# Kernel tuning notes

Measured on AMD Instinct MI355X. Metric: run time of the kernel, lower is better.

Reference implementation:

```python
import jax, jax.numpy as jnp
import numpy as np

N_NODES = 50000
N_EDGES = 800000
N_GRAPHS = 256
F_IN, HID, EMB = 128, 256, 128
N_GROUPS, N_FAM = 16, 128


def setup_inputs() -> dict:
    key = jax.random.key(0)
    ks = jax.random.split(key, 12)
    x = jax.random.normal(ks[0], (N_NODES, F_IN), dtype=jnp.float32)
    edge_index = jax.random.randint(ks[1], (2, N_EDGES), 0, N_NODES, dtype=jnp.int64)
    batch = jnp.sort(jax.random.randint(ks[2], (N_NODES,), 0, N_GRAPHS, dtype=jnp.int64))
    def lin(k, fi, fo):
        s = 1.0 / np.sqrt(fi)
        return jax.random.uniform(k, (fi, fo), minval=-s, maxval=s, dtype=jnp.float32)
    W1 = lin(ks[3], F_IN, HID); b1 = jnp.zeros((HID,), jnp.float32)
    W2 = lin(ks[4], HID, EMB); b2 = jnp.zeros((EMB,), jnp.float32)
    Wg = lin(ks[5], EMB, N_GROUPS); bg = jnp.zeros((N_GROUPS,), jnp.float32)
    s = 1.0 / np.sqrt(EMB)
    Wf = jax.random.uniform(ks[6], (N_GROUPS, EMB, N_FAM), minval=-s, maxval=s, dtype=jnp.float32)
    bf = jnp.zeros((N_GROUPS, N_FAM), jnp.float32)
    return {"x": x, "edge_index": edge_index, "batch": batch,
            "W1": W1, "b1": b1, "W2": W2, "b2": b2,
            "Wg": Wg, "bg": bg, "Wf": Wf, "bf": bf}


def _gcn_conv(h, src, dst, coef, W, b, n):
    # h: [N, Fin]; src/dst: [E'] (self-loops included); coef: [E'] sym-norm
    hw = h @ W                                    # [N, Fout]
    msg = hw[src] * coef[:, None]                 # gather + scale, [E', Fout]
    out = jax.ops.segment_sum(msg, dst, num_segments=n)  # scatter-add
    return out + b


def reference(x, edge_index, batch, W1, b1, W2, b2, Wg, bg, Wf, bf):
    n = x.shape[0]
    loops = jnp.arange(n, dtype=edge_index.dtype)
    src = jnp.concatenate([edge_index[0], loops])
    dst = jnp.concatenate([edge_index[1], loops])
    # symmetric GCN normalization (deg >= 1 thanks to self-loops)
    deg = jax.ops.segment_sum(jnp.ones_like(dst, dtype=x.dtype), dst, num_segments=n)
    dinv = jax.lax.rsqrt(deg)
    coef = dinv[src] * dinv[dst]

    h1 = jax.nn.relu(_gcn_conv(x, src, dst, coef, W1, b1, n))  # dropout = identity (eval)
    h2 = _gcn_conv(h1, src, dst, coef, W2, b2, n)

    # global mean pool over graphs
    sums = jax.ops.segment_sum(h2, batch, num_segments=N_GRAPHS)
    cnts = jax.ops.segment_sum(jnp.ones((n,), x.dtype), batch, num_segments=N_GRAPHS)
    embeddings = sums / jnp.maximum(cnts, 1.0)[:, None]        # [G, EMB]

    group_logits = embeddings @ Wg + bg                        # [G, n_groups]
    pred_groups = jnp.argmax(group_logits, axis=1)             # routing
    # per-graph routed family classifier (dense equivalent of the dict outputs)
    family_logits = jnp.einsum('gd,gdf->gf', embeddings, Wf[pred_groups]) + bf[pred_groups]
    return embeddings, group_logits, family_logits
```

## Files before the change

kernel.cpp:

```cpp
#include <hip/hip_runtime.h>
#include <hip/hip_fp16.h>
#include <cstddef>
#include <cstdint>

static constexpr int NN   = 50000;
static constexpr int NE   = 800000;
static constexpr int NG   = 256;
static constexpr int FIN  = 128;
static constexpr int HID  = 256;
static constexpr int EMB  = 128;
static constexpr int NGRP = 16;
static constexpr int NFAM = 128;
static constexpr int NETOT = NE + NN;

static constexpr int SCAN_B  = 256;
static constexpr int SCAN_CH = (NN + SCAN_B - 1) / SCAN_B;

static constexpr int NSLICE  = 8;
static constexpr int SLICE_W = (NN + NSLICE - 1) / NSLICE;
static constexpr int BUILD_RANKS = 64;

using bf16x8 = __attribute__((ext_vector_type(8))) short;
using f32x4  = __attribute__((ext_vector_type(4))) float;

__device__ __forceinline__ unsigned short f2bf(float f) {
    uint32_t u = __float_as_uint(f);
    u += 0x7FFFu + ((u >> 16) & 1u);
    return (unsigned short)(u >> 16);
}
__device__ __forceinline__ float bf2f(unsigned short u) {
    return __uint_as_float((uint32_t)u << 16);
}
__device__ __forceinline__ void unpack_sw(uint32_t v, int& s, float& w) {
    s = (int)(v & 0xFFFFu);
    w = __half2float(__ushort_as_half((unsigned short)(v >> 16)));
}


__global__ void k_count(const int* __restrict__ esrc, const int* __restrict__ edst,
                        int* __restrict__ degi, uint32_t* __restrict__ sdpack, int e) {
    int i = blockIdx.x * blockDim.x + threadIdx.x;
    if (i < e) {
        int d = edst[i];
        int s = esrc[i];
        atomicAdd(degi + d, 1);
        sdpack[i] = ((uint32_t)d << 16) | (uint32_t)s;
    }
}

__global__ void k_prep(const int* __restrict__ degi, const int* __restrict__ batch,
                       float* __restrict__ dinv, int* __restrict__ gstart,
                       float* __restrict__ emb_acc, int n, int G) {
    int i = blockIdx.x * blockDim.x + threadIdx.x;
    if (i < NG * EMB) emb_acc[i] = 0.f;
    if (i >= n) return;
    dinv[i] = rsqrtf((float)(degi[i] + 1));
    int b  = batch[i];
    int pb = (i == 0) ? -1 : batch[i - 1];
    for (int g = pb + 1; g <= b; ++g) gstart[g] = i;
    if (i == n - 1) {
        for (int g = b + 1; g <= G; ++g) gstart[g] = n;
    }
}

__global__ void k_xconv(const float* __restrict__ x, const float* __restrict__ dinv,
                        unsigned short* __restrict__ xs) {
    int t = blockIdx.x * blockDim.x + threadIdx.x;
    size_t i = (size_t)t * 8;
    float dv = dinv[t >> 4];
    float4 a = *(const float4*)(x + i);
    float4 b = *(const float4*)(x + i + 4);
    uint4 o;
    o.x = (uint32_t)f2bf(dv * a.x) | ((uint32_t)f2bf(dv * a.y) << 16);
    o.y = (uint32_t)f2bf(dv * a.z) | ((uint32_t)f2bf(dv * a.w) << 16);
    o.z = (uint32_t)f2bf(dv * b.x) | ((uint32_t)f2bf(dv * b.y) << 16);
    o.w = (uint32_t)f2bf(dv * b.z) | ((uint32_t)f2bf(dv * b.w) << 16);
    *(uint4*)(xs + i) = o;
}

__global__ void k_wconv(const float* __restrict__ W1, const float* __restrict__ W2,
                        unsigned short* __restrict__ W1t, unsigned short* __restrict__ W2t) {
    int t = blockIdx.x * blockDim.x + threadIdx.x;
    if (t < HID * FIN) {
        int nidx = t >> 7, k = t & 127;
        W1t[t] = f2bf(W1[(size_t)k * HID + nidx]);
    } else {
        int u = t - HID * FIN;
        int nidx = u >> 8, k = u & 255;
        W2t[u] = f2bf(W2[(size_t)k * EMB + nidx]);
    }
}


__global__ __launch_bounds__(256) void k_scanA(const int* __restrict__ degi,
                                               const int* __restrict__ gstart,
                                               float* __restrict__ rcnt,
                                               int* __restrict__ row_ptr,
                                               int* __restrict__ bsum, int n) {
    const int b = blockIdx.x, t = threadIdx.x;
    if (b == 0 && t < NG) {
        int c = gstart[t + 1] - gstart[t];
        rcnt[t] = 1.0f / (float)max(c, 1);
    }
    __shared__ int sh[256];
    const int idx = b * SCAN_CH + t;
    int v = 0;
    if (t < SCAN_CH && idx < n) v = degi[idx] + 1;
    sh[t] = v;
    __syncthreads();
    for (int off = 1; off < 256; off <<= 1) {
        int y = (t >= off) ? sh[t - off] : 0;
        __syncthreads();
        if (t >= off) sh[t] += y;
        __syncthreads();
    }
    if (t < SCAN_CH && idx < n) row_ptr[idx] = sh[t] - v;
    if (t == 255) bsum[b] = sh[255];
}

__global__ __launch_bounds__(256) void k_scanB(const int* __restrict__ bsum,
                                               const int* __restrict__ batch,
                                               const float* __restrict__ dinv,
                                               const float* __restrict__ rcnt,
                                               int* __restrict__ row_ptr,
                                               unsigned long long* __restrict__ combo,
                                               int n) {
    __shared__ int sh[SCAN_B];
    const int b = blockIdx.x, t = threadIdx.x;
    sh[t] = bsum[t];
    __syncthreads();
    for (int off = 1; off < SCAN_B; off <<= 1) {
        int y = (t >= off) ? sh[t - off] : 0;
        __syncthreads();
        if (t >= off) sh[t] += y;
        __syncthreads();
    }
    const int boff = (b == 0) ? 0 : sh[b - 1];
    const int idx  = b * SCAN_CH + t;
    if (t < SCAN_CH && idx < n) {
        int rp = row_ptr[idx] + boff;
        row_ptr[idx] = rp;
        unsigned short wh = __half_as_ushort(
            __float2half(dinv[idx] * rcnt[batch[idx]]));
        combo[idx] = ((unsigned long long)wh << 32) | (unsigned int)(rp + 1);
    }
    if (b == 0 && t == 0) row_ptr[n] = sh[SCAN_B - 1];
}


__global__ __launch_bounds__(256) void k_build(
        const uint32_t* __restrict__ sdpack, const int* __restrict__ row_ptr,
        unsigned long long* __restrict__ combo, uint32_t* __restrict__ eP,
        int n, int e) {
    const int slice = blockIdx.x & 7;
    const int rank  = blockIdx.x >> 3;
    const int lo = slice * SLICE_W;
    const int hi = min(lo + SLICE_W, n);
    for (int i = lo + rank * 256 + (int)threadIdx.x; i < hi; i += BUILD_RANKS * 256) {
        uint32_t rp = (uint32_t)row_ptr[i];
        uint32_t wh = (uint32_t)(combo[i] >> 32) & 0xFFFFu;
        eP[rp] = (uint32_t)i | (wh << 16);
    }
    for (int j = rank * 256 + (int)threadIdx.x; j < e; j += BUILD_RANKS * 256) {
        uint32_t p = __builtin_nontemporal_load(sdpack + j);
        int d = (int)(p >> 16);
        if (d < lo || d >= hi) continue;
        unsigned long long old = atomicAdd(combo + d, 1ull);
        eP[(uint32_t)old] = (p & 0xFFFFu) | (((uint32_t)(old >> 32) & 0xFFFFu) << 16);
    }
}


__global__ __launch_bounds__(256) void k_agg(
        const unsigned short* __restrict__ xs, const int* __restrict__ row_ptr,
        const uint32_t* __restrict__ eP, const float* __restrict__ dinv,
        unsigned short* __restrict__ xa, int n) {
    int node = blockIdx.x * 4 + (threadIdx.x >> 6);
    if (node >= n) return;
    int lane = threadIdx.x & 63;
    int grp = lane >> 4, fl = lane & 15;
    float acc[8] = {};
    int beg = row_ptr[node], end = row_ptr[node + 1];
    for (int j = beg; j < end; j += 4) {
        int jj = j + grp;
        bool valid = jj < end;
        uint32_t ev = __builtin_nontemporal_load(eP + (valid ? jj : beg));
        int s = (int)(ev & 0xFFFFu);
        float m = valid ? 1.f : 0.f;
        bf16x8 v = *(const bf16x8*)(xs + ((size_t)s << 7) + fl * 8);
#pragma unroll
        for (int k = 0; k < 8; ++k)
            acc[k] += m * bf2f((unsigned short)v[k]);
    }
#pragma unroll
    for (int k = 0; k < 8; ++k) {
        acc[k] += __shfl_xor(acc[k], 16);
        acc[k] += __shfl_xor(acc[k], 32);
    }
    if (lane < 16) {
        float di = dinv[node];
        uint4 o;
        o.x = (uint32_t)f2bf(di * acc[0]) | ((uint32_t)f2bf(di * acc[1]) << 16);
        o.y = (uint32_t)f2bf(di * acc[2]) | ((uint32_t)f2bf(di * acc[3]) << 16);
        o.z = (uint32_t)f2bf(di * acc[4]) | ((uint32_t)f2bf(di * acc[5]) << 16);
        o.w = (uint32_t)f2bf(di * acc[6]) | ((uint32_t)f2bf(di * acc[7]) << 16);
        *(uint4*)(xa + ((size_t)node << 7) + fl * 8) = o;
    }
}


__global__ __launch_bounds__(256) void k_fgemm(
        const unsigned short* __restrict__ A,
        const unsigned short* __restrict__ W1t,
        const unsigned short* __restrict__ W2t,
        const float* __restrict__ b1, const float* __restrict__ dinv,
        unsigned short* __restrict__ H, int M) {
    __shared__ unsigned short h1s[64 * 256];
    const int m0 = blockIdx.x * 64;
    const int w  = threadIdx.x >> 6;
    const int l  = threadIdx.x & 63;
    const int lr = l & 15;
    const int lk = l >> 4;

    {
        f32x4 acc[4][4] = {};
        const int n0 = w * 64;
#pragma unroll
        for (int ks = 0; ks < 4; ++ks) {
            const int k0 = ks * 32 + lk * 8;
            bf16x8 bfr[4];
#pragma unroll
            for (int ni = 0; ni < 4; ++ni)
                bfr[ni] = *(const bf16x8*)(W1t + (size_t)(n0 + ni * 16 + lr) * FIN + k0);
#pragma unroll
            for (int mi = 0; mi < 4; ++mi) {
                int row = min(m0 + mi * 16 + lr, M - 1);
                bf16x8 afr = *(const bf16x8*)(A + ((size_t)row << 7) + k0);
#pragma unroll
                for (int ni = 0; ni < 4; ++ni)
                    acc[mi][ni] = __builtin_amdgcn_mfma_f32_16x16x32_bf16(
                        afr, bfr[ni], acc[mi][ni], 0, 0, 0);
            }
        }
#pragma unroll
        for (int ni = 0; ni < 4; ++ni) {
            int col = n0 + ni * 16 + lr;
            float bb = b1[col];
#pragma unroll
            for (int mi = 0; mi < 4; ++mi) {
#pragma unroll
                for (int r = 0; r < 4; ++r) {
                    int rl = mi * 16 + lk * 4 + r;
                    float dv = dinv[min(m0 + rl, M - 1)];
                    float v = fmaxf(acc[mi][ni][r] + bb, 0.f) * dv;
                    int byte = (rl * 512 + col * 2) ^ ((rl & 7) << 4);
                    *(unsigned short*)((char*)h1s + byte) = f2bf(v);
                }
            }
        }
    }
    __syncthreads();
    f32x4 acc2[4][2] = {};
    {
        const int n0 = w * 32;
#pragma unroll
        for (int ks = 0; ks < 8; ++ks) {
            const int k0 = ks * 32 + lk * 8;
            bf16x8 bfr[2];
#pragma unroll
            for (int ni = 0; ni < 2; ++ni)
                bfr[ni] = *(const bf16x8*)(W2t + (size_t)(n0 + ni * 16 + lr) * HID + k0);
#pragma unroll
            for (int mi = 0; mi < 4; ++mi) {
                int rl = mi * 16 + lr;
                int byte = (rl * 512 + k0 * 2) ^ ((rl & 7) << 4);
                bf16x8 afr = *(const bf16x8*)((const char*)h1s + byte);
#pragma unroll
                for (int ni = 0; ni < 2; ++ni)
                    acc2[mi][ni] = __builtin_amdgcn_mfma_f32_16x16x32_bf16(
                        afr, bfr[ni], acc2[mi][ni], 0, 0, 0);
            }
        }
    }
    __syncthreads();
    {
        const int n0 = w * 32;
#pragma unroll
        for (int ni = 0; ni < 2; ++ni) {
            int col = n0 + ni * 16 + lr;
#pragma unroll
            for (int mi = 0; mi < 4; ++mi)
#pragma unroll
                for (int r = 0; r < 4; ++r) {
                    int rl = mi * 16 + lk * 4 + r;
                    h1s[rl * EMB + col] = f2bf(acc2[mi][ni][r]);
                }
        }
    }
    __syncthreads();
    int nrows = min(64, M - m0);
    for (int c = threadIdx.x; c < nrows * 16; c += 256) {
        int rl = c >> 4, cc = c & 15;
        *(uint4*)(H + ((size_t)(m0 + rl) << 7) + cc * 8) =
            *(const uint4*)(h1s + rl * EMB + cc * 8);
    }
}


__global__ __launch_bounds__(256) void k_pool(
        const unsigned short* __restrict__ H, const int* __restrict__ row_ptr,
        const int* __restrict__ gstart, const uint32_t* __restrict__ eP,
        float* __restrict__ emb_acc) {
    __shared__ float red[4][EMB];
    const int g  = blockIdx.x >> 3;
    const int kb = blockIdx.x & 7;
    const int e0 = row_ptr[gstart[g]];
    const int e1 = row_ptr[gstart[g + 1]];
    const int len = e1 - e0;
    const int per = (len + 7) >> 3;
    const int s0  = e0 + kb * per;
    const int s1  = min(s0 + per, e1);
    const int lane = threadIdx.x & 63;
    const int wv   = threadIdx.x >> 6;
    const int grp = lane >> 4, fl = lane & 15;

    float acc[8] = {};
    for (int j = s0 + wv * 4; j < s1; j += 16) {
        int jj = j + grp;
        bool valid = jj < s1;
        uint32_t ev = __builtin_nontemporal_load(eP + (valid ? jj : s0));
        int s; float wgt;
        unpack_sw(ev, s, wgt);
        if (!valid) wgt = 0.f;
        bf16x8 v = *(const bf16x8*)(H + ((size_t)s << 7) + fl * 8);
#pragma unroll
        for (int k = 0; k < 8; ++k)
            acc[k] += wgt * bf2f((unsigned short)v[k]);
    }
#pragma unroll
    for (int k = 0; k < 8; ++k) {
        acc[k] += __shfl_xor(acc[k], 16);
        acc[k] += __shfl_xor(acc[k], 32);
    }
    if (lane < 16) {
#pragma unroll
        for (int k = 0; k < 8; ++k) red[wv][fl * 8 + k] = acc[k];
    }
    __syncthreads();
    int t = threadIdx.x;
    if (t < EMB) {
        float v = red[0][t] + red[1][t] + red[2][t] + red[3][t];
        if (v != 0.f) atomicAdd(&emb_acc[g * EMB + t], v);
    }
}


__global__ __launch_bounds__(128) void k_head(const float* __restrict__ emb_acc,
                                              const int* __restrict__ gstart,
                                              const float* __restrict__ b2,
                                              const float* __restrict__ Wg,
                                              const float* __restrict__ bg,
                                              const float* __restrict__ Wf,
                                              const float* __restrict__ bff,
                                              float* __restrict__ out_emb,
                                              float* __restrict__ out_gl,
                                              float* __restrict__ out_fl) {
    __shared__ float e[EMB];
    __shared__ float gl[NGRP];
    __shared__ int ps;
    int g = blockIdx.x, c = threadIdx.x;
    bool nonempty = gstart[g + 1] > gstart[g];
    float a = emb_acc[g * EMB + c] + (nonempty ? b2[c] : 0.f);
    e[c] = a;
    out_emb[(size_t)g * EMB + c] = a;
    __syncthreads();
    if (c < NGRP) {
        float s = bg[c];
        for (int d = 0; d < EMB; ++d) s += e[d] * Wg[d * NGRP + c];
        gl[c] = s;
        out_gl[g * NGRP + c] = s;
    }
    __syncthreads();
    if (c == 0) {
        int bi = 0;
        float bv = gl[0];
        for (int t2 = 1; t2 < NGRP; ++t2)
            if (gl[t2] > bv) { bv = gl[t2]; bi = t2; }
        ps = bi;
    }
    __syncthreads();
    int pr = ps;
    float s = bff[pr * NFAM + c];
    for (int d = 0; d < EMB; ++d) s += e[d] * Wf[((size_t)pr * EMB + d) * NFAM + c];
    out_fl[g * NFAM + c] = s;
}


extern "C" void kernel_launch(void* const* d_in, const int* in_sizes, int n_in,
                              void* d_out, int out_size, void* d_ws, size_t ws_size,
                              hipStream_t stream) {
    const float* x   = (const float*)d_in[0];
    const int*   ei  = (const int*)d_in[1];
    const int*   bat = (const int*)d_in[2];
    const float* W1  = (const float*)d_in[3];
    const float* b1  = (const float*)d_in[4];
    const float* W2  = (const float*)d_in[5];
    const float* b2  = (const float*)d_in[6];
    const float* Wg  = (const float*)d_in[7];
    const float* bg  = (const float*)d_in[8];
    const float* Wf  = (const float*)d_in[9];
    const float* bf  = (const float*)d_in[10];

    float* out     = (float*)d_out;
    float* out_emb = out;
    float* out_gl  = out + (size_t)NG * EMB;
    float* out_fl  = out_gl + (size_t)NG * NGRP;

    char* w = (char*)d_ws;
    auto alloc = [&](size_t bytes) {
        char* p = w;
        w += (bytes + 255) & ~(size_t)255;
        return p;
    };
    int*                 degi    = (int*)alloc((size_t)NN * 4);
    float*               dinv    = (float*)alloc((size_t)NN * 4);
    int*                 row_ptr = (int*)alloc((size_t)(NN + 1) * 4);
    unsigned long long*  combo   = (unsigned long long*)alloc((size_t)NN * 8);
    int*                 bsum    = (int*)alloc((size_t)SCAN_B * 4);
    uint32_t*            sdpack  = (uint32_t*)alloc((size_t)NE * 4);
    uint32_t*            eP      = (uint32_t*)alloc((size_t)NETOT * 4);
    int*                 gstart  = (int*)alloc((size_t)(NG + 1) * 4);
    float*               rcnt    = (float*)alloc((size_t)NG * 4);
    unsigned short*      xs      = (unsigned short*)alloc((size_t)NN * FIN * 2);
    unsigned short*      xa      = (unsigned short*)alloc((size_t)NN * FIN * 2);
    unsigned short*      W1t     = (unsigned short*)alloc((size_t)HID * FIN * 2);
    unsigned short*      W2t     = (unsigned short*)alloc((size_t)EMB * HID * 2);
    unsigned short*      H       = (unsigned short*)alloc((size_t)NN * EMB * 2);
    float*               emb_acc = (float*)alloc((size_t)NG * EMB * 4);

    const int* esrc = ei;
    const int* edst = ei + NE;

    hipMemsetAsync(degi, 0, (size_t)NN * 4, stream);
    k_count<<<(NE + 255) / 256, 256, 0, stream>>>(esrc, edst, degi, sdpack, NE);
    k_prep<<<(NG * HID + 255) / 256, 256, 0, stream>>>(degi, bat, dinv, gstart,
                                                       emb_acc, NN, NG);
    k_xconv<<<(NN * 16) / 256, 256, 0, stream>>>(x, dinv, xs);
    k_wconv<<<(HID * FIN + EMB * HID) / 256, 256, 0, stream>>>(W1, W2, W1t, W2t);
    k_scanA<<<SCAN_B, 256, 0, stream>>>(degi, gstart, rcnt, row_ptr, bsum, NN);
    k_scanB<<<SCAN_B, 256, 0, stream>>>(bsum, bat, dinv, rcnt, row_ptr, combo, NN);
    k_build<<<NSLICE * BUILD_RANKS, 256, 0, stream>>>(sdpack, row_ptr, combo, eP, NN, NE);

    k_agg<<<(NN + 3) / 4, 256, 0, stream>>>(xs, row_ptr, eP, dinv, xa, NN);
    k_fgemm<<<(NN + 63) / 64, 256, 0, stream>>>(xa, W1t, W2t, b1, dinv, H, NN);

    k_pool<<<NG * 8, 256, 0, stream>>>(H, row_ptr, gstart, eP, emb_acc);

    k_head<<<NG, 128, 0, stream>>>(emb_acc, gstart, b2, Wg, bg, Wf, bf,
                                   out_emb, out_gl, out_fl);
}
```

Before: 226.3 us.

## Shrink CSR to 16-bit indices, fuse setup kernels, move dinv scaling to gather

```diff
diff --git a/kernel.cpp b/kernel.cpp
--- a/kernel.cpp
+++ b/kernel.cpp
@@ -20,6 +20,10 @@
 static constexpr int SLICE_W = (NN + NSLICE - 1) / NSLICE;
 static constexpr int BUILD_RANKS = 64;
 
+static constexpr int SETUP_B_CNT = (NE + 255) / 256;
+static constexpr int SETUP_B_X   = (NN * FIN / 8 + 255) / 256;
+static constexpr int SETUP_B_W   = (HID * FIN + EMB * HID) / 256;
+
 using bf16x8 = __attribute__((ext_vector_type(8))) short;
 using f32x4  = __attribute__((ext_vector_type(4))) float;
 
@@ -31,20 +35,47 @@
 __device__ __forceinline__ float bf2f(unsigned short u) {
     return __uint_as_float((uint32_t)u << 16);
 }
-__device__ __forceinline__ void unpack_sw(uint32_t v, int& s, float& w) {
-    s = (int)(v & 0xFFFFu);
-    w = __half2float(__ushort_as_half((unsigned short)(v >> 16)));
-}
-
-
-__global__ void k_count(const int* __restrict__ esrc, const int* __restrict__ edst,
-                        int* __restrict__ degi, uint32_t* __restrict__ sdpack, int e) {
-    int i = blockIdx.x * blockDim.x + threadIdx.x;
-    if (i < e) {
-        int d = edst[i];
-        int s = esrc[i];
-        atomicAdd(degi + d, 1);
-        sdpack[i] = ((uint32_t)d << 16) | (uint32_t)s;
+
+
+__global__ __launch_bounds__(256) void k_setup(
+        const int* __restrict__ esrc, const int* __restrict__ edst,
+        const float* __restrict__ x, const float* __restrict__ W1,
+        const float* __restrict__ W2, int* __restrict__ degi,
+        uint32_t* __restrict__ sdpack, unsigned short* __restrict__ xs,
+        unsigned short* __restrict__ W1t, unsigned short* __restrict__ W2t) {
+    int b = blockIdx.x;
+    if (b < SETUP_B_CNT) {
+        int i = b * 256 + threadIdx.x;
+        if (i < NE) {
+            int d = edst[i];
+            int s = esrc[i];
+            atomicAdd(degi + d, 1);
+            sdpack[i] = ((uint32_t)d << 16) | (uint32_t)s;
+        }
+        return;
+    }
+    b -= SETUP_B_CNT;
+    if (b < SETUP_B_X) {
+        size_t i = ((size_t)b * 256 + threadIdx.x) * 8;
+        float4 a = *(const float4*)(x + i);
+        float4 c = *(const float4*)(x + i + 4);
+        uint4 o;
+        o.x = (uint32_t)f2bf(a.x) | ((uint32_t)f2bf(a.y) << 16);
+        o.y = (uint32_t)f2bf(a.z) | ((uint32_t)f2bf(a.w) << 16);
+        o.z = (uint32_t)f2bf(c.x) | ((uint32_t)f2bf(c.y) << 16);
+        o.w = (uint32_t)f2bf(c.z) | ((uint32_t)f2bf(c.w) << 16);
+        *(uint4*)(xs + i) = o;
+        return;
+    }
+    b -= SETUP_B_X;
+    int t = b * 256 + threadIdx.x;
+    if (t < HID * FIN) {
+        int nidx = t >> 7, k = t & 127;
+        W1t[t] = f2bf(W1[(size_t)k * HID + nidx]);
+    } else {
+        int u = t - HID * FIN;
+        int nidx = u >> 8, k = u & 255;
+        W2t[u] = f2bf(W2[(size_t)k * EMB + nidx]);
     }
 }
 
@@ -63,34 +94,6 @@
     }
 }
 
-__global__ void k_xconv(const float* __restrict__ x, const float* __restrict__ dinv,
-                        unsigned short* __restrict__ xs) {
-    int t = blockIdx.x * blockDim.x + threadIdx.x;
-    size_t i = (size_t)t * 8;
-    float dv = dinv[t >> 4];
-    float4 a = *(const float4*)(x + i);
-    float4 b = *(const float4*)(x + i + 4);
-    uint4 o;
-    o.x = (uint32_t)f2bf(dv * a.x) | ((uint32_t)f2bf(dv * a.y) << 16);
-    o.y = (uint32_t)f2bf(dv * a.z) | ((uint32_t)f2bf(dv * a.w) << 16);
-    o.z = (uint32_t)f2bf(dv * b.x) | ((uint32_t)f2bf(dv * b.y) << 16);
-    o.w = (uint32_t)f2bf(dv * b.z) | ((uint32_t)f2bf(dv * b.w) << 16);
-    *(uint4*)(xs + i) = o;
-}
-
-__global__ void k_wconv(const float* __restrict__ W1, const float* __restrict__ W2,
-                        unsigned short* __restrict__ W1t, unsigned short* __restrict__ W2t) {
-    int t = blockIdx.x * blockDim.x + threadIdx.x;
-    if (t < HID * FIN) {
-        int nidx = t >> 7, k = t & 127;
-        W1t[t] = f2bf(W1[(size_t)k * HID + nidx]);
-    } else {
-        int u = t - HID * FIN;
-        int nidx = u >> 8, k = u & 255;
-        W2t[u] = f2bf(W2[(size_t)k * EMB + nidx]);
-    }
-}
-
 
 __global__ __launch_bounds__(256) void k_scanA(const int* __restrict__ degi,
                                                const int* __restrict__ gstart,
@@ -119,11 +122,9 @@
 }
 
 __global__ __launch_bounds__(256) void k_scanB(const int* __restrict__ bsum,
-                                               const int* __restrict__ batch,
-                                               const float* __restrict__ dinv,
-                                               const float* __restrict__ rcnt,
                                                int* __restrict__ row_ptr,
-                                               unsigned long long* __restrict__ combo,
+                                               int* __restrict__ cursor,
+                                               unsigned short* __restrict__ eP16,
                                                int n) {
     __shared__ int sh[SCAN_B];
     const int b = blockIdx.x, t = threadIdx.x;
@@ -140,40 +141,33 @@
     if (t < SCAN_CH && idx < n) {
         int rp = row_ptr[idx] + boff;
         row_ptr[idx] = rp;
-        unsigned short wh = __half_as_ushort(
-            __float2half(dinv[idx] * rcnt[batch[idx]]));
-        combo[idx] = ((unsigned long long)wh << 32) | (unsigned int)(rp + 1);
+        cursor[idx]  = rp + 1;
+        eP16[rp] = (unsigned short)idx;
     }
     if (b == 0 && t == 0) row_ptr[n] = sh[SCAN_B - 1];
 }
 
 
 __global__ __launch_bounds__(256) void k_build(
-        const uint32_t* __restrict__ sdpack, const int* __restrict__ row_ptr,
-        unsigned long long* __restrict__ combo, uint32_t* __restrict__ eP,
-        int n, int e) {
+        const uint32_t* __restrict__ sdpack, int* __restrict__ cursor,
+        unsigned short* __restrict__ eP16, int n, int e) {
     const int slice = blockIdx.x & 7;
-    const int rank  = blockIdx.x >> 3;
     const int lo = slice * SLICE_W;
     const int hi = min(lo + SLICE_W, n);
-    for (int i = lo + rank * 256 + (int)threadIdx.x; i < hi; i += BUILD_RANKS * 256) {
-        uint32_t rp = (uint32_t)row_ptr[i];
-        uint32_t wh = (uint32_t)(combo[i] >> 32) & 0xFFFFu;
-        eP[rp] = (uint32_t)i | (wh << 16);
-    }
+    const int rank = blockIdx.x >> 3;
     for (int j = rank * 256 + (int)threadIdx.x; j < e; j += BUILD_RANKS * 256) {
         uint32_t p = __builtin_nontemporal_load(sdpack + j);
         int d = (int)(p >> 16);
         if (d < lo || d >= hi) continue;
-        unsigned long long old = atomicAdd(combo + d, 1ull);
-        eP[(uint32_t)old] = (p & 0xFFFFu) | (((uint32_t)(old >> 32) & 0xFFFFu) << 16);
+        int slot = atomicAdd(cursor + d, 1);
+        eP16[slot] = (unsigned short)(p & 0xFFFFu);
     }
 }
 
 
 __global__ __launch_bounds__(256) void k_agg(
         const unsigned short* __restrict__ xs, const int* __restrict__ row_ptr,
-        const uint32_t* __restrict__ eP, const float* __restrict__ dinv,
+        const unsigned short* __restrict__ eP16, const float* __restrict__ dinv,
         unsigned short* __restrict__ xa, int n) {
     int node = blockIdx.x * 4 + (threadIdx.x >> 6);
     if (node >= n) return;
@@ -184,9 +178,8 @@
     for (int j = beg; j < end; j += 4) {
         int jj = j + grp;
         bool valid = jj < end;
-        uint32_t ev = __builtin_nontemporal_load(eP + (valid ? jj : beg));
-        int s = (int)(ev & 0xFFFFu);
-        float m = valid ? 1.f : 0.f;
+        int s = (int)__builtin_nontemporal_load(eP16 + (valid ? jj : beg));
+        float m = valid ? dinv[s] : 0.f;
         bf16x8 v = *(const bf16x8*)(xs + ((size_t)s << 7) + fl * 8);
 #pragma unroll
         for (int k = 0; k < 8; ++k)
@@ -309,33 +302,30 @@
 
 __global__ __launch_bounds__(256) void k_pool(
         const unsigned short* __restrict__ H, const int* __restrict__ row_ptr,
-        const int* __restrict__ gstart, const uint32_t* __restrict__ eP,
-        float* __restrict__ emb_acc) {
+        const int* __restrict__ gstart, const unsigned short* __restrict__ eP16,
+        const float* __restrict__ dinv, float* __restrict__ emb_acc) {
     __shared__ float red[4][EMB];
     const int g  = blockIdx.x >> 3;
     const int kb = blockIdx.x & 7;
-    const int e0 = row_ptr[gstart[g]];
-    const int e1 = row_ptr[gstart[g + 1]];
-    const int len = e1 - e0;
-    const int per = (len + 7) >> 3;
-    const int s0  = e0 + kb * per;
-    const int s1  = min(s0 + per, e1);
+    const int n0 = gstart[g], n1 = gstart[g + 1];
     const int lane = threadIdx.x & 63;
     const int wv   = threadIdx.x >> 6;
     const int grp = lane >> 4, fl = lane & 15;
 
     float acc[8] = {};
-    for (int j = s0 + wv * 4; j < s1; j += 16) {
-        int jj = j + grp;
-        bool valid = jj < s1;
-        uint32_t ev = __builtin_nontemporal_load(eP + (valid ? jj : s0));
-        int s; float wgt;
-        unpack_sw(ev, s, wgt);
-        if (!valid) wgt = 0.f;
-        bf16x8 v = *(const bf16x8*)(H + ((size_t)s << 7) + fl * 8);
-#pragma unroll
-        for (int k = 0; k < 8; ++k)
-            acc[k] += wgt * bf2f((unsigned short)v[k]);
+    for (int d = n0 + kb * 4 + wv; d < n1; d += 32) {
+        int beg = row_ptr[d], end = row_ptr[d + 1];
+        float dd = dinv[d];
+        for (int j = beg; j < end; j += 4) {
+            int jj = j + grp;
+            bool valid = jj < end;
+            int s = (int)__builtin_nontemporal_load(eP16 + (valid ? jj : beg));
+            float m = valid ? dd : 0.f;
+            bf16x8 v = *(const bf16x8*)(H + ((size_t)s << 7) + fl * 8);
+#pragma unroll
+            for (int k = 0; k < 8; ++k)
+                acc[k] += m * bf2f((unsigned short)v[k]);
+        }
     }
 #pragma unroll
     for (int k = 0; k < 8; ++k) {
@@ -357,6 +347,7 @@
 
 __global__ __launch_bounds__(128) void k_head(const float* __restrict__ emb_acc,
                                               const int* __restrict__ gstart,
+                                              const float* __restrict__ rcnt,
                                               const float* __restrict__ b2,
                                               const float* __restrict__ Wg,
                                               const float* __restrict__ bg,
@@ -370,7 +361,7 @@
     __shared__ int ps;
     int g = blockIdx.x, c = threadIdx.x;
     bool nonempty = gstart[g + 1] > gstart[g];
-    float a = emb_acc[g * EMB + c] + (nonempty ? b2[c] : 0.f);
+    float a = emb_acc[g * EMB + c] * rcnt[g] + (nonempty ? b2[c] : 0.f);
     e[c] = a;
     out_emb[(size_t)g * EMB + c] = a;
     __syncthreads();
@@ -422,40 +413,39 @@
         w += (bytes + 255) & ~(size_t)255;
         return p;
     };
-    int*                 degi    = (int*)alloc((size_t)NN * 4);
-    float*               dinv    = (float*)alloc((size_t)NN * 4);
-    int*                 row_ptr = (int*)alloc((size_t)(NN + 1) * 4);
-    unsigned long long*  combo   = (unsigned long long*)alloc((size_t)NN * 8);
-    int*                 bsum    = (int*)alloc((size_t)SCAN_B * 4);
-    uint32_t*            sdpack  = (uint32_t*)alloc((size_t)NE * 4);
-    uint32_t*            eP      = (uint32_t*)alloc((size_t)NETOT * 4);
-    int*                 gstart  = (int*)alloc((size_t)(NG + 1) * 4);
-    float*               rcnt    = (float*)alloc((size_t)NG * 4);
-    unsigned short*      xs      = (unsigned short*)alloc((size_t)NN * FIN * 2);
-    unsigned short*      xa      = (unsigned short*)alloc((size_t)NN * FIN * 2);
-    unsigned short*      W1t     = (unsigned short*)alloc((size_t)HID * FIN * 2);
-    unsigned short*      W2t     = (unsigned short*)alloc((size_t)EMB * HID * 2);
-    unsigned short*      H       = (unsigned short*)alloc((size_t)NN * EMB * 2);
-    float*               emb_acc = (float*)alloc((size_t)NG * EMB * 4);
+    int*             degi    = (int*)alloc((size_t)NN * 4);
+    float*           dinv    = (float*)alloc((size_t)NN * 4);
+    int*             row_ptr = (int*)alloc((size_t)(NN + 1) * 4);
+    int*             cursor  = (int*)alloc((size_t)NN * 4);
+    int*             bsum    = (int*)alloc((size_t)SCAN_B * 4);
+    uint32_t*        sdpack  = (uint32_t*)alloc((size_t)NE * 4);
+    unsigned short*  eP16    = (unsigned short*)alloc((size_t)NETOT * 2);
+    int*             gstart  = (int*)alloc((size_t)(NG + 1) * 4);
+    float*           rcnt    = (float*)alloc((size_t)NG * 4);
+    unsigned short*  xs      = (unsigned short*)alloc((size_t)NN * FIN * 2);
+    unsigned short*  xa      = (unsigned short*)alloc((size_t)NN * FIN * 2);
+    unsigned short*  W1t     = (unsigned short*)alloc((size_t)HID * FIN * 2);
+    unsigned short*  W2t     = (unsigned short*)alloc((size_t)EMB * HID * 2);
+    unsigned short*  H       = (unsigned short*)alloc((size_t)NN * EMB * 2);
+    float*           emb_acc = (float*)alloc((size_t)NG * EMB * 4);
 
     const int* esrc = ei;
     const int* edst = ei + NE;
 
     hipMemsetAsync(degi, 0, (size_t)NN * 4, stream);
-    k_count<<<(NE + 255) / 256, 256, 0, stream>>>(esrc, edst, degi, sdpack, NE);
+    k_setup<<<SETUP_B_CNT + SETUP_B_X + SETUP_B_W, 256, 0, stream>>>(
+        esrc, edst, x, W1, W2, degi, sdpack, xs, W1t, W2t);
     k_prep<<<(NG * HID + 255) / 256, 256, 0, stream>>>(degi, bat, dinv, gstart,
                                                        emb_acc, NN, NG);
-    k_xconv<<<(NN * 16) / 256, 256, 0, stream>>>(x, dinv, xs);
-    k_wconv<<<(HID * FIN + EMB * HID) / 256, 256, 0, stream>>>(W1, W2, W1t, W2t);
     k_scanA<<<SCAN_B, 256, 0, stream>>>(degi, gstart, rcnt, row_ptr, bsum, NN);
-    k_scanB<<<SCAN_B, 256, 0, stream>>>(bsum, bat, dinv, rcnt, row_ptr, combo, NN);
-    k_build<<<NSLICE * BUILD_RANKS, 256, 0, stream>>>(sdpack, row_ptr, combo, eP, NN, NE);
-
-    k_agg<<<(NN + 3) / 4, 256, 0, stream>>>(xs, row_ptr, eP, dinv, xa, NN);
+    k_scanB<<<SCAN_B, 256, 0, stream>>>(bsum, row_ptr, cursor, eP16, NN);
+    k_build<<<NSLICE * BUILD_RANKS, 256, 0, stream>>>(sdpack, cursor, eP16, NN, NE);
+
+    k_agg<<<(NN + 3) / 4, 256, 0, stream>>>(xs, row_ptr, eP16, dinv, xa, NN);
     k_fgemm<<<(NN + 63) / 64, 256, 0, stream>>>(xa, W1t, W2t, b1, dinv, H, NN);
 
-    k_pool<<<NG * 8, 256, 0, stream>>>(H, row_ptr, gstart, eP, emb_acc);
-
-    k_head<<<NG, 128, 0, stream>>>(emb_acc, gstart, b2, Wg, bg, Wf, bf,
+    k_pool<<<NG * 8, 256, 0, stream>>>(H, row_ptr, gstart, eP16, dinv, emb_acc);
+
+    k_head<<<NG, 128, 0, stream>>>(emb_acc, gstart, rcnt, b2, Wg, bg, Wf, bf,
                                    out_emb, out_gl, out_fl);
 }
```

Result: slower. 236.5 us (+4.5%).
